# Kernel tuning notes

Measured on AMD Instinct MI355X. Metric: run time of the kernel, lower is better.

## Reference

```python
import jax, jax.numpy as jnp
import numpy as np


def setup_inputs() -> dict:
    key = jax.random.key(0)
    ks = jax.random.split(key, 5)
    B, Lq, Lkv, HQ, H, D, S, BS = 1, 256, 4096, 32, 2, 128, 16, 64
    q = jax.random.normal(ks[0], (B, Lq, HQ, D), jnp.float32)
    k = jax.random.normal(ks[1], (B, Lkv, H, D), jnp.float32)
    v = jax.random.normal(ks[2], (B, Lkv, H, D), jnp.float32)
    w = jax.random.uniform(ks[3], (B, Lq, HQ, S), jnp.float32)
    block_indices = jax.random.randint(ks[4], (B, Lq, H, S), 0, Lkv // BS).astype(jnp.int32)
    return {"q": q, "k": k, "v": v, "w": w, "block_indices": block_indices, "block_size": BS}


def reference(q, k, v, w, block_indices, block_size):
    # q: (B, Lq, HQ, D); k,v: (B, Lkv, H, D); w: (B, Lq, HQ, num_weights);
    # block_indices: (B, Lq, H, S) int32, entries < 0 are skipped.
    B, Lq, HQ, D = q.shape
    H = k.shape[2]
    S = block_indices.shape[-1]
    G = HQ // H  # query heads per kv head
    nb = k.shape[1] // block_size
    sm_scale = 1.0 / (D ** 0.5)  # default scale in the kernel

    # Reshape KV into blocks: (B, H, nb, BS, D)
    kb = k.reshape(B, nb, block_size, H, D).transpose(0, 3, 1, 2, 4)
    vb = v.reshape(B, nb, block_size, H, D).transpose(0, 3, 1, 2, 4)

    idx = block_indices.transpose(0, 2, 1, 3)  # (B, H, Lq, S)
    valid = idx >= 0
    idx = jnp.maximum(idx, 0)

    # Gather selected blocks per (batch, kv_head): -> (B, H, Lq, S, BS, D)
    gather = jax.vmap(jax.vmap(lambda blocks, ind: blocks[ind]))
    kg = gather(kb, idx)
    vg = gather(vb, idx)

    # Group query heads by kv head: (B, H, Lq, G, D)
    qh = q.reshape(B, Lq, H, G, D).transpose(0, 2, 1, 3, 4)

    # Per-block scores and per-block softmax over the BS keys (axis u)
    scores = jnp.einsum('bhlgd,bhlsud->bhlgsu', qh, kg) * sm_scale
    p = jax.nn.softmax(scores, axis=-1)

    # Per-(head, block) learned weight; only first S weights of w are used.
    wh = w[..., :S].reshape(B, Lq, H, G, S).transpose(0, 2, 1, 3, 4)  # (B,H,Lq,G,S)
    coef = wh * valid[:, :, :, None, :].astype(p.dtype)
    p = p * coef[..., None]

    o = jnp.einsum('bhlgsu,bhlsud->bhlgd', p, vg)  # (B, H, Lq, G, D)
    return o.transpose(0, 2, 1, 3, 4).reshape(B, Lq, HQ, D)
```

## Files before the change

### kernel.cpp

```cpp
#include <hip/hip_runtime.h>
#include <hip/hip_bf16.h>


namespace {

constexpr int kLq = 256, kHQ = 32, kH = 2, kG = 16, kD = 128, kS = 16;
constexpr int kNB = 64;
constexpr float kScaleLog2e = 0.08838834764831845f * 1.4426950408889634f;

constexpr int kKPackN = kH * kNB * 16 * 64;
constexpr int kPStr   = 72;
constexpr int kSStr   = 136;

typedef short s16x8 __attribute__((ext_vector_type(8)));
typedef float f32x4 __attribute__((ext_vector_type(4)));

union U32BF2 { unsigned int u; __hip_bfloat162 h; };

static __device__ inline unsigned int pk_bf16(float a, float b) {
    U32BF2 z; z.h = __float22bfloat162_rn(make_float2(a, b));
    return z.u;
}

__global__ __launch_bounds__(256)
void pack_kv(const float* __restrict__ k, const float* __restrict__ v,
             uint4* __restrict__ kp, uint4* __restrict__ vp)
{
    __shared__ unsigned short S_s[64 * kSStr];

    const int bid  = blockIdx.x;
    const int isV  = bid & 1;
    const int blk  = (bid >> 1) & 63;
    const int h    = bid >> 7;
    const int t    = threadIdx.x;
    const int lane = t & 63, n = lane & 15, quad = lane >> 4;
    const int wv   = t >> 6;

    {
        const float* src = (isV ? v : k) + ((size_t)blk * 64 * kH + h) * kD;
        const int r0 = t >> 5, c4 = (t & 31) << 2;
        #pragma unroll
        for (int p = 0; p < 8; ++p) {
            const int r = p * 8 + r0;
            const float4 f = *(const float4*)(src + (size_t)r * (kH * kD) + c4);
            *(unsigned int*)&S_s[r * kSStr + c4]     = pk_bf16(f.x, f.y);
            *(unsigned int*)&S_s[r * kSStr + c4 + 2] = pk_bf16(f.z, f.w);
        }
    }
    __syncthreads();

    const size_t obase = (size_t)(h * 64 + blk) * 16 * 64;
    if (!isV) {
        #pragma unroll
        for (int rep = 0; rep < 4; ++rep) {
            const int u = wv * 16 + n;
            kp[obase + (size_t)(wv * 4 + rep) * 64 + lane] =
                *(const uint4*)&S_s[u * kSStr + rep * 32 + quad * 8];
        }
    } else {
        #pragma unroll
        for (int rep = 0; rep < 4; ++rep) {
            const int c  = wv * 4 + rep;
            const int d  = (c >> 1) * 16 + n;
            const int u0 = (c & 1) * 32 + quad * 8;
            unsigned short s[8];
            #pragma unroll
            for (int j = 0; j < 8; ++j) s[j] = S_s[(u0 + j) * kSStr + d];
            uint4 val;
            val.x = s[0] | ((unsigned)s[1] << 16);
            val.y = s[2] | ((unsigned)s[3] << 16);
            val.z = s[4] | ((unsigned)s[5] << 16);
            val.w = s[6] | ((unsigned)s[7] << 16);
            vp[obase + (size_t)c * 64 + lane] = val;
        }
    }
}

__global__ __launch_bounds__(256, 2)
void hsa_main(const float* __restrict__ q, const float* __restrict__ w,
              const int* __restrict__ bidx, const uint4* __restrict__ kp,
              const uint4* __restrict__ vp, float* __restrict__ out)
{
    __shared__ __align__(16) uint4 buf[2][32 * 64];
    __shared__ __align__(16) unsigned short P_s[4 * kG * kPStr];

    const int bid  = blockIdx.x;
    const int l    = bid >> 1;
    const int h    = bid & 1;
    const int tid  = threadIdx.x;
    const int wave = tid >> 6;
    const int lane = tid & 63;
    const int n    = lane & 15;
    const int quad = lane >> 4;

    s16x8 qf[4];
    {
        const float* qb = q + ((size_t)l * kHQ + h * kG + n) * kD + quad * 8;
        #pragma unroll
        for (int st = 0; st < 4; ++st) {
            const float4 f0 = *(const float4*)(qb + st * 32);
            const float4 f1 = *(const float4*)(qb + st * 32 + 4);
            union { s16x8 v; unsigned int u[4]; } z;
            z.u[0] = pk_bf16(f0.x, f0.y); z.u[1] = pk_bf16(f0.z, f0.w);
            z.u[2] = pk_bf16(f1.x, f1.y); z.u[3] = pk_bf16(f1.z, f1.w);
            qf[st] = z.v;
        }
    }

    int   base_[kS];
    float wval[kS];
    #pragma unroll
    for (int i = 0; i < 4; ++i) {
        const int4   b4 = *(const int4*)(bidx + (size_t)(l * kH + h) * kS + i * 4);
        const float4 w4 = *(const float4*)(w + ((size_t)l * kHQ + h * kG + n) * kS + i * 4);
        const int   bb[4] = {b4.x, b4.y, b4.z, b4.w};
        const float ww[4] = {w4.x, w4.y, w4.z, w4.w};
        #pragma unroll
        for (int jj = 0; jj < 4; ++jj) {
            wval[i * 4 + jj]  = (bb[jj] < 0) ? 0.f : ww[jj];
            base_[i * 4 + jj] = (h * kNB + max(bb[jj], 0)) * 1024;
        }
    }

    const int    f0    = wave * 8;
    const uint4* gsrc  = (f0 < 16) ? kp : vp;
    const int    fbase = (f0 < 16) ? f0 * 64 : (f0 - 16) * 64;

    #define STAGE(js_, b_)                                                     \
        {                                                                      \
            const uint4* gp = gsrc + base_[(js_)] + fbase + lane;              \
            auto* lp = (__attribute__((address_space(3))) uint4*)&buf[(b_)][f0 * 64]; \
            _Pragma("unroll")                                                  \
            for (int i_ = 0; i_ < 8; ++i_)                                     \
                __builtin_amdgcn_global_load_lds(                              \
                    (const __attribute__((address_space(1))) void*)(gp + i_ * 64), \
                    (__attribute__((address_space(3))) void*)(lp + i_ * 64),   \
                    16, 0, 0);                                                 \
        }

    STAGE(0, 0);
    __syncthreads();

    unsigned short* Pw = &P_s[wave * kG * kPStr];
    f32x4 oacc0 = {0.f, 0.f, 0.f, 0.f};
    f32x4 oacc1 = {0.f, 0.f, 0.f, 0.f};

    #pragma unroll
    for (int js = 0; js < kS; ++js) {
        const int cur = js & 1;

        if (js < kS - 1) {
            STAGE(js + 1, cur ^ 1);
            __builtin_amdgcn_sched_barrier(0);
        }

        f32x4 sc[4];
        #pragma unroll
        for (int t = 0; t < 4; ++t) sc[t] = (f32x4){0.f, 0.f, 0.f, 0.f};
        #pragma unroll
        for (int t = 0; t < 4; ++t)
            #pragma unroll
            for (int st = 0; st < 4; ++st) {
                const s16x8 af = *(const s16x8*)&buf[cur][(t * 4 + st) * 64 + lane];
                sc[t] = __builtin_amdgcn_mfma_f32_16x16x32_bf16(af, qf[st], sc[t], 0, 0, 0);
            }

        float part = 0.f;
        #pragma unroll
        for (int t = 0; t < 4; ++t)
            #pragma unroll
            for (int r = 0; r < 4; ++r) {
                sc[t][r] = exp2f(sc[t][r] * kScaleLog2e);
                part += sc[t][r];
            }
        part += __shfl_xor(part, 16);
        part += __shfl_xor(part, 32);
        const float coef = wval[js] / part;

        #pragma unroll
        for (int t = 0; t < 4; ++t) {
            const unsigned long long pq =
                ((unsigned long long)pk_bf16(sc[t][2] * coef, sc[t][3] * coef) << 32) |
                pk_bf16(sc[t][0] * coef, sc[t][1] * coef);
            *(unsigned long long*)&Pw[n * kPStr + t * 16 + quad * 4] = pq;
        }
        const s16x8 bf0 = *(const s16x8*)&Pw[n * kPStr + quad * 8];
        const s16x8 bf1 = *(const s16x8*)&Pw[n * kPStr + 32 + quad * 8];

        {
            const int dt0 = wave * 2;
            const s16x8 a00 = *(const s16x8*)&buf[cur][(16 + dt0 * 2 + 0) * 64 + lane];
            const s16x8 a01 = *(const s16x8*)&buf[cur][(16 + dt0 * 2 + 1) * 64 + lane];
            oacc0 = __builtin_amdgcn_mfma_f32_16x16x32_bf16(a00, bf0, oacc0, 0, 0, 0);
            oacc0 = __builtin_amdgcn_mfma_f32_16x16x32_bf16(a01, bf1, oacc0, 0, 0, 0);
            const s16x8 a10 = *(const s16x8*)&buf[cur][(16 + dt0 * 2 + 2) * 64 + lane];
            const s16x8 a11 = *(const s16x8*)&buf[cur][(16 + dt0 * 2 + 3) * 64 + lane];
            oacc1 = __builtin_amdgcn_mfma_f32_16x16x32_bf16(a10, bf0, oacc1, 0, 0, 0);
            oacc1 = __builtin_amdgcn_mfma_f32_16x16x32_bf16(a11, bf1, oacc1, 0, 0, 0);
        }

        __syncthreads();
    }
    #undef STAGE

    {
        float* ob = out + ((size_t)l * kHQ + h * kG + n) * kD;
        const int d0 = wave * 32 + quad * 4;
        *(float4*)(ob + d0)      = make_float4(oacc0[0], oacc0[1], oacc0[2], oacc0[3]);
        *(float4*)(ob + d0 + 16) = make_float4(oacc1[0], oacc1[1], oacc1[2], oacc1[3]);
    }
}

}

extern "C" void kernel_launch(void* const* d_in, const int* in_sizes, int n_in,
                              void* d_out, int out_size, void* d_ws, size_t ws_size,
                              hipStream_t stream)
{
    const float* q    = (const float*)d_in[0];
    const float* k    = (const float*)d_in[1];
    const float* v    = (const float*)d_in[2];
    const float* w    = (const float*)d_in[3];
    const int*   bidx = (const int*)d_in[4];
    float* out = (float*)d_out;

    uint4* kp = (uint4*)d_ws;
    uint4* vp = (uint4*)((char*)d_ws + (size_t)kKPackN * 16);

    pack_kv<<<dim3(256), dim3(256), 0, stream>>>(k, v, kp, vp);
    hsa_main<<<dim3(kLq * kH), dim3(256), 0, stream>>>(q, w, bidx, kp, vp, out);
}
```

Before: 102.1 us.

## Split QK^T across waves with K in registers and cross-wave softmax sums

Each wave now computes scores for its own 16 keys of the block, with K fragments loaded straight into registers and prefetched one block ahead. Only V is staged through LDS, and each wave owns a D slice. Per-wave partial softmax sums are exchanged through shared memory, and the normalisation coefficient is applied after the PV MFMA. This removes the QK^T work every wave previously duplicated and halves LDS use so occupancy can rise to 3 blocks per SIMD. The pack kernel is also split into half-blocks to double its grid. The cost is an extra shared-memory exchange before the PV step.

```diff
diff --git a/kernel.cpp b/kernel.cpp
--- a/kernel.cpp
+++ b/kernel.cpp
@@ -16,6 +16,7 @@
 typedef float f32x4 __attribute__((ext_vector_type(4)));
 
 union U32BF2 { unsigned int u; __hip_bfloat162 h; };
+union FragU  { uint4 u; s16x8 v; };
 
 static __device__ inline unsigned int pk_bf16(float a, float b) {
     U32BF2 z; z.h = __float22bfloat162_rn(make_float2(a, b));
@@ -26,21 +27,23 @@
 void pack_kv(const float* __restrict__ k, const float* __restrict__ v,
              uint4* __restrict__ kp, uint4* __restrict__ vp)
 {
-    __shared__ unsigned short S_s[64 * kSStr];
+    __shared__ unsigned short S_s[32 * kSStr];
 
     const int bid  = blockIdx.x;
     const int isV  = bid & 1;
-    const int blk  = (bid >> 1) & 63;
-    const int h    = bid >> 7;
+    const int half = (bid >> 1) & 1;
+    const int blk  = (bid >> 2) & 63;
+    const int h    = bid >> 8;
     const int t    = threadIdx.x;
     const int lane = t & 63, n = lane & 15, quad = lane >> 4;
     const int wv   = t >> 6;
 
     {
-        const float* src = (isV ? v : k) + ((size_t)blk * 64 * kH + h) * kD;
+        const float* src = (isV ? v : k) +
+            ((size_t)(blk * 64 + half * 32) * kH + h) * kD;
         const int r0 = t >> 5, c4 = (t & 31) << 2;
         #pragma unroll
-        for (int p = 0; p < 8; ++p) {
+        for (int p = 0; p < 4; ++p) {
             const int r = p * 8 + r0;
             const float4 f = *(const float4*)(src + (size_t)r * (kH * kD) + c4);
             *(unsigned int*)&S_s[r * kSStr + c4]     = pk_bf16(f.x, f.y);
@@ -52,20 +55,23 @@
     const size_t obase = (size_t)(h * 64 + blk) * 16 * 64;
     if (!isV) {
         #pragma unroll
-        for (int rep = 0; rep < 4; ++rep) {
-            const int u = wv * 16 + n;
-            kp[obase + (size_t)(wv * 4 + rep) * 64 + lane] =
-                *(const uint4*)&S_s[u * kSStr + rep * 32 + quad * 8];
+        for (int rep = 0; rep < 2; ++rep) {
+            const int cl    = wv * 2 + rep;
+            const int t_loc = cl >> 2, st = cl & 3;
+            const int c     = (2 * half + t_loc) * 4 + st;
+            const int u_loc = t_loc * 16 + n;
+            kp[obase + (size_t)c * 64 + lane] =
+                *(const uint4*)&S_s[u_loc * kSStr + st * 32 + quad * 8];
         }
     } else {
         #pragma unroll
-        for (int rep = 0; rep < 4; ++rep) {
-            const int c  = wv * 4 + rep;
-            const int d  = (c >> 1) * 16 + n;
-            const int u0 = (c & 1) * 32 + quad * 8;
+        for (int rep = 0; rep < 2; ++rep) {
+            const int dt = wv * 2 + rep;
+            const int c  = dt * 2 + half;
+            const int d  = dt * 16 + n;
             unsigned short s[8];
             #pragma unroll
-            for (int j = 0; j < 8; ++j) s[j] = S_s[(u0 + j) * kSStr + d];
+            for (int j = 0; j < 8; ++j) s[j] = S_s[(quad * 8 + j) * kSStr + d];
             uint4 val;
             val.x = s[0] | ((unsigned)s[1] << 16);
             val.y = s[2] | ((unsigned)s[3] << 16);
@@ -76,13 +82,14 @@
     }
 }
 
-__global__ __launch_bounds__(256, 2)
+__global__ __launch_bounds__(256, 3)
 void hsa_main(const float* __restrict__ q, const float* __restrict__ w,
               const int* __restrict__ bidx, const uint4* __restrict__ kp,
               const uint4* __restrict__ vp, float* __restrict__ out)
 {
-    __shared__ __align__(16) uint4 buf[2][32 * 64];
-    __shared__ __align__(16) unsigned short P_s[4 * kG * kPStr];
+    __shared__ __align__(16) uint4 vbuf[2][16 * 64];
+    __shared__ __align__(16) unsigned short P_s[2][kG * kPStr];
+    __shared__ __align__(16) float psum[2][kG][4];
 
     const int bid  = blockIdx.x;
     const int l    = bid >> 1;
@@ -122,26 +129,26 @@
         }
     }
 
-    const int    f0    = wave * 8;
-    const uint4* gsrc  = (f0 < 16) ? kp : vp;
-    const int    fbase = (f0 < 16) ? f0 * 64 : (f0 - 16) * 64;
-
-    #define STAGE(js_, b_)                                                     \
+    #define STAGE_V(js_, b_)                                                   \
         {                                                                      \
-            const uint4* gp = gsrc + base_[(js_)] + fbase + lane;              \
-            auto* lp = (__attribute__((address_space(3))) uint4*)&buf[(b_)][f0 * 64]; \
+            const uint4* gp = vp + base_[(js_)] + (wave * 4) * 64 + lane;      \
+            auto* lp = (__attribute__((address_space(3))) uint4*)              \
+                           &vbuf[(b_)][(wave * 4) * 64];                       \
             _Pragma("unroll")                                                  \
-            for (int i_ = 0; i_ < 8; ++i_)                                     \
+            for (int i_ = 0; i_ < 4; ++i_)                                     \
                 __builtin_amdgcn_global_load_lds(                              \
                     (const __attribute__((address_space(1))) void*)(gp + i_ * 64), \
                     (__attribute__((address_space(3))) void*)(lp + i_ * 64),   \
                     16, 0, 0);                                                 \
         }
 
-    STAGE(0, 0);
-    __syncthreads();
-
-    unsigned short* Pw = &P_s[wave * kG * kPStr];
+    STAGE_V(0, 0);
+    FragU kreg[4];
+    #pragma unroll
+    for (int st = 0; st < 4; ++st)
+        kreg[st].u = kp[base_[0] + (wave * 4 + st) * 64 + lane];
+    __builtin_amdgcn_sched_barrier(0);
+
     f32x4 oacc0 = {0.f, 0.f, 0.f, 0.f};
     f32x4 oacc1 = {0.f, 0.f, 0.f, 0.f};
 
@@ -149,59 +156,58 @@
     for (int js = 0; js < kS; ++js) {
         const int cur = js & 1;
 
+        f32x4 sc = {0.f, 0.f, 0.f, 0.f};
+        #pragma unroll
+        for (int st = 0; st < 4; ++st)
+            sc = __builtin_amdgcn_mfma_f32_16x16x32_bf16(kreg[st].v, qf[st], sc, 0, 0, 0);
+
         if (js < kS - 1) {
-            STAGE(js + 1, cur ^ 1);
-            __builtin_amdgcn_sched_barrier(0);
-        }
-
-        f32x4 sc[4];
-        #pragma unroll
-        for (int t = 0; t < 4; ++t) sc[t] = (f32x4){0.f, 0.f, 0.f, 0.f};
-        #pragma unroll
-        for (int t = 0; t < 4; ++t)
             #pragma unroll
-            for (int st = 0; st < 4; ++st) {
-                const s16x8 af = *(const s16x8*)&buf[cur][(t * 4 + st) * 64 + lane];
-                sc[t] = __builtin_amdgcn_mfma_f32_16x16x32_bf16(af, qf[st], sc[t], 0, 0, 0);
-            }
+            for (int st = 0; st < 4; ++st)
+                kreg[st].u = kp[base_[js + 1] + (wave * 4 + st) * 64 + lane];
+        }
+        __builtin_amdgcn_sched_barrier(0);
 
         float part = 0.f;
         #pragma unroll
-        for (int t = 0; t < 4; ++t)
-            #pragma unroll
-            for (int r = 0; r < 4; ++r) {
-                sc[t][r] = exp2f(sc[t][r] * kScaleLog2e);
-                part += sc[t][r];
-            }
+        for (int r = 0; r < 4; ++r) {
+            sc[r] = exp2f(sc[r] * kScaleLog2e);
+            part += sc[r];
+        }
         part += __shfl_xor(part, 16);
         part += __shfl_xor(part, 32);
-        const float coef = wval[js] / part;
-
-        #pragma unroll
-        for (int t = 0; t < 4; ++t) {
-            const unsigned long long pq =
-                ((unsigned long long)pk_bf16(sc[t][2] * coef, sc[t][3] * coef) << 32) |
-                pk_bf16(sc[t][0] * coef, sc[t][1] * coef);
-            *(unsigned long long*)&Pw[n * kPStr + t * 16 + quad * 4] = pq;
-        }
-        const s16x8 bf0 = *(const s16x8*)&Pw[n * kPStr + quad * 8];
-        const s16x8 bf1 = *(const s16x8*)&Pw[n * kPStr + 32 + quad * 8];
-
-        {
-            const int dt0 = wave * 2;
-            const s16x8 a00 = *(const s16x8*)&buf[cur][(16 + dt0 * 2 + 0) * 64 + lane];
-            const s16x8 a01 = *(const s16x8*)&buf[cur][(16 + dt0 * 2 + 1) * 64 + lane];
-            oacc0 = __builtin_amdgcn_mfma_f32_16x16x32_bf16(a00, bf0, oacc0, 0, 0, 0);
-            oacc0 = __builtin_amdgcn_mfma_f32_16x16x32_bf16(a01, bf1, oacc0, 0, 0, 0);
-            const s16x8 a10 = *(const s16x8*)&buf[cur][(16 + dt0 * 2 + 2) * 64 + lane];
-            const s16x8 a11 = *(const s16x8*)&buf[cur][(16 + dt0 * 2 + 3) * 64 + lane];
-            oacc1 = __builtin_amdgcn_mfma_f32_16x16x32_bf16(a10, bf0, oacc1, 0, 0, 0);
-            oacc1 = __builtin_amdgcn_mfma_f32_16x16x32_bf16(a11, bf1, oacc1, 0, 0, 0);
-        }
+        if (quad == 0) psum[cur][n][wave] = part;
+
+        const unsigned long long pq =
+            ((unsigned long long)pk_bf16(sc[2], sc[3]) << 32) | pk_bf16(sc[0], sc[1]);
+        *(unsigned long long*)&P_s[cur][n * kPStr + wave * 16 + quad * 4] = pq;
 
         __syncthreads();
-    }
-    #undef STAGE
+
+        const float4 ps  = *(const float4*)&psum[cur][n][0];
+        const float coef = wval[js] / (ps.x + ps.y + ps.z + ps.w);
+        const s16x8 bf0 = *(const s16x8*)&P_s[cur][n * kPStr + quad * 8];
+        const s16x8 bf1 = *(const s16x8*)&P_s[cur][n * kPStr + 32 + quad * 8];
+
+        if (js < kS - 1) { STAGE_V(js + 1, cur ^ 1); }
+        __builtin_amdgcn_sched_barrier(0);
+
+        const f32x4 zero = {0.f, 0.f, 0.f, 0.f};
+        const s16x8 a0 = *(const s16x8*)&vbuf[cur][(wave * 4 + 0) * 64 + lane];
+        const s16x8 a1 = *(const s16x8*)&vbuf[cur][(wave * 4 + 1) * 64 + lane];
+        const s16x8 a2 = *(const s16x8*)&vbuf[cur][(wave * 4 + 2) * 64 + lane];
+        const s16x8 a3 = *(const s16x8*)&vbuf[cur][(wave * 4 + 3) * 64 + lane];
+        f32x4 p0 = __builtin_amdgcn_mfma_f32_16x16x32_bf16(a0, bf0, zero, 0, 0, 0);
+        p0       = __builtin_amdgcn_mfma_f32_16x16x32_bf16(a1, bf1, p0,   0, 0, 0);
+        f32x4 p1 = __builtin_amdgcn_mfma_f32_16x16x32_bf16(a2, bf0, zero, 0, 0, 0);
+        p1       = __builtin_amdgcn_mfma_f32_16x16x32_bf16(a3, bf1, p1,   0, 0, 0);
+        #pragma unroll
+        for (int r = 0; r < 4; ++r) {
+            oacc0[r] = fmaf(coef, p0[r], oacc0[r]);
+            oacc1[r] = fmaf(coef, p1[r], oacc1[r]);
+        }
+    }
+    #undef STAGE_V
 
     {
         float* ob = out + ((size_t)l * kHQ + h * kG + n) * kD;
@@ -227,6 +233,6 @@
     uint4* kp = (uint4*)d_ws;
     uint4* vp = (uint4*)((char*)d_ws + (size_t)kKPackN * 16);
 
-    pack_kv<<<dim3(256), dim3(256), 0, stream>>>(k, v, kp, vp);
+    pack_kv<<<dim3(512), dim3(256), 0, stream>>>(k, v, kp, vp);
     hsa_main<<<dim3(kLq * kH), dim3(256), 0, stream>>>(q, w, bidx, kp, vp, out);
 }
```

Result: faster. 97.12 us (-4.9%).
